# Optimization experiments

Measured on AMD Instinct MI355X. Metric: run time of the kernel, lower is better.

Reference implementation:

```python
import jax, jax.numpy as jnp
import numpy as np

N_NODES, N_EDGES, CH, FEAT = 20000, 320000, 256, 118


def setup_inputs() -> dict:
    key = jax.random.key(0)
    ks = jax.random.split(key, 8)
    x = jax.random.uniform(ks[0], (N_NODES, FEAT), dtype=jnp.float32)
    edge_index = jax.random.randint(ks[1], (2, N_EDGES), 0, N_NODES, dtype=jnp.int64)
    s = 0.05
    W_embed = jax.random.normal(ks[2], (FEAT, CH), dtype=jnp.float32) * s
    b_embed = jnp.zeros((CH,), jnp.float32)
    W1 = jax.random.normal(ks[3], (CH, CH), dtype=jnp.float32) * s
    b1 = jnp.zeros((CH,), jnp.float32)
    W2 = jax.random.normal(ks[4], (CH, CH), dtype=jnp.float32) * s
    b2 = jnp.zeros((CH,), jnp.float32)
    return {"x": x, "edge_index": edge_index, "W_embed": W_embed, "b_embed": b_embed,
            "W1": W1, "b1": b1, "W2": W2, "b2": b2}


def reference(x, edge_index, W_embed, b_embed, W1, b1, W2, b2):
    n = x.shape[0]
    # node embedding: Linear(118 -> C)
    h = x @ W_embed + b_embed  # [N, C]
    src, dst = edge_index[0], edge_index[1]
    # message: gather x_j per edge, dense1 + exact GELU (dropout = identity in eval)
    msg = jax.nn.gelu(h[src] @ W1 + b1, approximate=False)  # [E, C]
    # mean aggregation into destination nodes
    agg = jax.ops.segment_sum(msg, dst, num_segments=n)  # [N, C]
    cnt = jax.ops.segment_sum(jnp.ones((msg.shape[0],), msg.dtype), dst, num_segments=n)
    agg = agg / jnp.maximum(cnt, 1.0)[:, None]
    # update: dense2 + exact GELU
    out = jax.nn.gelu(agg @ W2 + b2, approximate=False)  # [N, C]
    # final mean over channel dim
    return out.mean(axis=1)  # [N]
```

## Files before the change

kernel.cpp:

```cpp
#include <hip/hip_runtime.h>
#include <math.h>

#define N_NODES 20000
#define N_EDGES 320000
#define CH      256
#define FEAT    118
#define CAP     48

typedef float    f32x4 __attribute__((ext_vector_type(4)));
typedef short    s16x8 __attribute__((ext_vector_type(8)));
typedef _Float16 f16x4 __attribute__((ext_vector_type(4)));
typedef _Float16 f16x8 __attribute__((ext_vector_type(8)));
typedef unsigned short u16;

union Frag  { s16x8 v; u16 u[8]; };
union FragH { f16x8 v; _Float16 h[8]; };

__device__ __forceinline__ float gelu_exact(float x) {
    return 0.5f * x * (1.0f + erff(x * 0.70710678118654752f));
}
__device__ __forceinline__ u16 f2bf(float f) {
    unsigned u = __float_as_uint(f);
    u = (u + 0x7FFFu + ((u >> 16) & 1u)) >> 16;
    return (u16)u;
}
__device__ __forceinline__ float bf2f(u16 h) { return __uint_as_float(((unsigned)h) << 16); }

__global__ __launch_bounds__(256) void prep(const float* __restrict__ x,
                                            const int* __restrict__ ei,
                                            const float* __restrict__ We,
                                            const float* __restrict__ be,
                                            const float* __restrict__ W1,
                                            const float* __restrict__ b1,
                                            const float* __restrict__ W2,
                                            u16* __restrict__ xh, u16* __restrict__ xl,
                                            int* __restrict__ cnt, int* __restrict__ bins,
                                            _Float16* __restrict__ w2h, _Float16* __restrict__ w2l,
                                            u16* __restrict__ wch, u16* __restrict__ wcl,
                                            float* __restrict__ bc) {
    const int b = blockIdx.x, tid = threadIdx.x;
    if (b < 1250) {
        __shared__ float xs[16][132];
        {
            int r = tid >> 4, ci = tid & 15;
            const float* xrow = x + (size_t)(b * 16 + r) * FEAT;
            #pragma unroll
            for (int it = 0; it < 8; it++) {
                int col = ci + it * 16;
                xs[r][col] = (col < FEAT) ? xrow[col] : 0.0f;
            }
        }
        __syncthreads();
        int lane = tid & 63, ks = tid >> 6;
        int row = lane & 15, k0 = ks * 32 + (lane >> 4) * 8;
        Frag hi, lo;
        #pragma unroll
        for (int j = 0; j < 8; j++) {
            float v = xs[row][k0 + j];
            u16 h = f2bf(v);
            hi.u[j] = h; lo.u[j] = f2bf(v - bf2f(h));
        }
        size_t fid = (size_t)b * 256 + tid;
        ((s16x8*)xh)[fid] = hi.v;
        ((s16x8*)xl)[fid] = lo.v;
    } else if (b < 2500) {
        int e = (b - 1250) * 256 + tid;
        int s = ei[e];
        int d = ei[N_EDGES + e];
        int p = atomicAdd(&cnt[d], 1);
        if (p < CAP) bins[(size_t)d * CAP + p] = s;
    } else if (b < 2532) {
        int fid = (b - 2500) * 256 + tid;
        int lane = fid & 63, ks = (fid >> 6) & 7, nt = fid >> 9;
        int n = nt * 16 + (lane & 15);
        int k0 = ks * 32 + (lane >> 4) * 8;
        FragH hi, lo;
        #pragma unroll
        for (int j = 0; j < 8; j++) {
            float v = W2[(size_t)(k0 + j) * 256 + n];
            _Float16 h = (_Float16)v;
            hi.h[j] = h;
            lo.h[j] = (_Float16)((v - (float)h) * 4096.0f);
        }
        ((f16x8*)w2h)[fid] = hi.v;
        ((f16x8*)w2l)[fid] = lo.v;
    } else {
        int f = b - 2532;
        int n = tid;
        if (f < 128) {
            float acc = 0.0f;
            if (f < FEAT) {
                const float* wr = We + (size_t)f * 256;
                #pragma unroll 8
                for (int c = 0; c < 256; c++) acc += wr[c] * W1[(size_t)c * 256 + n];
            }
            int nt = n >> 4, lm = n & 15, ks = f >> 5, q = (f >> 3) & 3, j = f & 7;
            size_t idx = (((size_t)nt * 4 + ks) * 64 + q * 16 + lm) * 8 + j;
            u16 h = f2bf(acc);
            wch[idx] = h;
            wcl[idx] = f2bf(acc - bf2f(h));
        } else {
            float acc = b1[n];
            #pragma unroll 8
            for (int c = 0; c < 256; c++) acc += be[c] * W1[(size_t)c * 256 + n];
            bc[n] = acc;
        }
    }
}

__global__ __launch_bounds__(256) void gemm_main(const u16* __restrict__ Ah_, const u16* __restrict__ Al_,
                                                 const u16* __restrict__ Bh_, const u16* __restrict__ Bl_,
                                                 const float* __restrict__ bias,
                                                 _Float16* __restrict__ Mout) {
    __shared__ _Float16 Ls[16][256];
    const int tid = threadIdx.x, wave = tid >> 6, lane = tid & 63;
    const int quad = lane >> 4, lm = lane & 15;
    const int mt = blockIdx.x, nt0 = wave * 4;
    const s16x8* Ah = (const s16x8*)Ah_; const s16x8* Al = (const s16x8*)Al_;
    const s16x8* Bh = (const s16x8*)Bh_; const s16x8* Bl = (const s16x8*)Bl_;
    f32x4 acc[4] = {f32x4{0,0,0,0}, f32x4{0,0,0,0}, f32x4{0,0,0,0}, f32x4{0,0,0,0}};
    #pragma unroll
    for (int ks = 0; ks < 4; ks++) {
        s16x8 a_h = Ah[((size_t)mt * 4 + ks) * 64 + lane];
        s16x8 a_l = Al[((size_t)mt * 4 + ks) * 64 + lane];
        #pragma unroll
        for (int t = 0; t < 4; t++) {
            s16x8 bh = Bh[((size_t)(nt0 + t) * 4 + ks) * 64 + lane];
            s16x8 bl = Bl[((size_t)(nt0 + t) * 4 + ks) * 64 + lane];
            acc[t] = __builtin_amdgcn_mfma_f32_16x16x32_bf16(a_h, bh, acc[t], 0, 0, 0);
            acc[t] = __builtin_amdgcn_mfma_f32_16x16x32_bf16(a_l, bh, acc[t], 0, 0, 0);
            acc[t] = __builtin_amdgcn_mfma_f32_16x16x32_bf16(a_h, bl, acc[t], 0, 0, 0);
        }
    }
    #pragma unroll
    for (int t = 0; t < 4; t++) {
        float bn = bias[(nt0 + t) * 16 + lm];
        #pragma unroll
        for (int r = 0; r < 4; r++)
            Ls[quad * 4 + r][(nt0 + t) * 16 + lm] = (_Float16)gelu_exact(acc[t][r] + bn);
    }
    __syncthreads();
    s16x8* dst = (s16x8*)Mout + (size_t)mt * 512;
    const s16x8* src = (const s16x8*)&Ls[0][0];
    dst[tid]       = src[tid];
    dst[256 + tid] = src[256 + tid];
}

__global__ __launch_bounds__(256) void aggregate(const _Float16* __restrict__ M,
                                                 const int* __restrict__ cnt,
                                                 const int* __restrict__ bins,
                                                 _Float16* __restrict__ aggf) {
    int node = (blockIdx.x * 256 + threadIdx.x) >> 6;
    int lane = threadIdx.x & 63;
    int c = cnt[node];
    int cc = min(c, CAP);
    int myid = (lane < CAP) ? bins[(size_t)node * CAP + lane] : 0;
    float a0 = 0.f, a1 = 0.f, a2 = 0.f, a3 = 0.f;
    for (int j = 0; j < cc; j += 8) {
        f16x4 v[8];
        #pragma unroll
        for (int u = 0; u < 8; u++) {
            int s = __shfl(myid, min(j + u, cc - 1), 64);
            v[u] = *(const f16x4*)(M + (size_t)s * CH + lane * 4);
        }
        #pragma unroll
        for (int u = 0; u < 8; u++) {
            if (j + u < cc) {
                a0 += (float)v[u].x; a1 += (float)v[u].y;
                a2 += (float)v[u].z; a3 += (float)v[u].w;
            }
        }
    }
    float inv = 1.0f / (float)max(c, 1);
    f16x4 o;
    o.x = (_Float16)(a0 * inv); o.y = (_Float16)(a1 * inv);
    o.z = (_Float16)(a2 * inv); o.w = (_Float16)(a3 * inv);
    int mt = node >> 4, lm = node & 15;
    int ks = lane >> 3, quad = (lane & 7) >> 1, j0 = (lane & 1) * 4;
    size_t base = (((size_t)mt * 8 + ks) * 64 + quad * 16 + lm) * 8 + j0;
    *(f16x4*)(aggf + base) = o;
}

__global__ __launch_bounds__(256) void gemm_mean(const _Float16* __restrict__ Af_,
                                                 const _Float16* __restrict__ Bh_, const _Float16* __restrict__ Bl_,
                                                 const float* __restrict__ bias,
                                                 float* __restrict__ out) {
    __shared__ float part[4][32];
    const int tid = threadIdx.x, wave = tid >> 6, lane = tid & 63;
    const int quad = lane >> 4, lm = lane & 15;
    const int mt0 = blockIdx.x * 2, nt0 = wave * 4;
    const f16x8* Af = (const f16x8*)Af_;
    const f16x8* Bh = (const f16x8*)Bh_; const f16x8* Bl = (const f16x8*)Bl_;
    f32x4 acch[2][4], accl[2][4];
    #pragma unroll
    for (int mi = 0; mi < 2; mi++)
        #pragma unroll
        for (int t = 0; t < 4; t++) {
            acch[mi][t] = f32x4{0.f, 0.f, 0.f, 0.f};
            accl[mi][t] = f32x4{0.f, 0.f, 0.f, 0.f};
        }
    #pragma unroll
    for (int ks = 0; ks < 8; ks++) {
        f16x8 a0 = Af[((size_t)(mt0 + 0) * 8 + ks) * 64 + lane];
        f16x8 a1 = Af[((size_t)(mt0 + 1) * 8 + ks) * 64 + lane];
        #pragma unroll
        for (int t = 0; t < 4; t++) {
            f16x8 bh = Bh[((size_t)(nt0 + t) * 8 + ks) * 64 + lane];
            f16x8 bl = Bl[((size_t)(nt0 + t) * 8 + ks) * 64 + lane];
            acch[0][t] = __builtin_amdgcn_mfma_f32_16x16x32_f16(a0, bh, acch[0][t], 0, 0, 0);
            accl[0][t] = __builtin_amdgcn_mfma_f32_16x16x32_f16(a0, bl, accl[0][t], 0, 0, 0);
            acch[1][t] = __builtin_amdgcn_mfma_f32_16x16x32_f16(a1, bh, acch[1][t], 0, 0, 0);
            accl[1][t] = __builtin_amdgcn_mfma_f32_16x16x32_f16(a1, bl, accl[1][t], 0, 0, 0);
        }
    }
    float p[2][4] = {{0.f,0.f,0.f,0.f},{0.f,0.f,0.f,0.f}};
    #pragma unroll
    for (int t = 0; t < 4; t++) {
        float bn = bias[(nt0 + t) * 16 + lm];
        #pragma unroll
        for (int mi = 0; mi < 2; mi++)
            #pragma unroll
            for (int r = 0; r < 4; r++)
                p[mi][r] += gelu_exact(acch[mi][t][r] + accl[mi][t][r] * (1.0f / 4096.0f) + bn);
    }
    #pragma unroll
    for (int off = 1; off < 16; off <<= 1)
        #pragma unroll
        for (int mi = 0; mi < 2; mi++)
            #pragma unroll
            for (int r = 0; r < 4; r++)
                p[mi][r] += __shfl_xor(p[mi][r], off, 64);
    if (lm == 0)
        #pragma unroll
        for (int mi = 0; mi < 2; mi++)
            #pragma unroll
            for (int r = 0; r < 4; r++)
                part[wave][mi * 16 + quad * 4 + r] = p[mi][r];
    __syncthreads();
    if (tid < 32) {
        float s = part[0][tid] + part[1][tid] + part[2][tid] + part[3][tid];
        out[blockIdx.x * 32 + tid] = s * (1.0f / 256.0f);
    }
}

extern "C" void kernel_launch(void* const* d_in, const int* in_sizes, int n_in,
                              void* d_out, int out_size, void* d_ws, size_t ws_size,
                              hipStream_t stream) {
    const float* x  = (const float*)d_in[0];
    const int*   ei = (const int*)d_in[1];
    const float* We = (const float*)d_in[2];
    const float* be = (const float*)d_in[3];
    const float* W1 = (const float*)d_in[4];
    const float* b1 = (const float*)d_in[5];
    const float* W2 = (const float*)d_in[6];
    const float* b2 = (const float*)d_in[7];
    float* out = (float*)d_out;

    char* ws = (char*)d_ws;
    size_t off = 0;
    u16* xh = (u16*)(ws + off);
    _Float16* aggf = (_Float16*)(ws + off);
    off += 5120000;
    u16* xl = (u16*)(ws + off); off += 5120000;
    _Float16* M = (_Float16*)(ws + off); off += 10240000;
    u16* wch = (u16*)(ws + off); off += 65536;
    u16* wcl = (u16*)(ws + off); off += 65536;
    _Float16* w2h = (_Float16*)(ws + off); off += 131072;
    _Float16* w2l = (_Float16*)(ws + off); off += 131072;
    float* bc = (float*)(ws + off); off += 1024;
    int* cnt  = (int*)(ws + off); off += N_NODES * 4;
    int* bins = (int*)(ws + off); off += (size_t)N_NODES * CAP * 4;

    hipMemsetAsync(cnt, 0, N_NODES * sizeof(int), stream);
    prep<<<2661, 256, 0, stream>>>(x, ei, We, be, W1, b1, W2,
                                   xh, xl, cnt, bins, w2h, w2l, wch, wcl, bc);
    gemm_main<<<N_NODES / 16, 256, 0, stream>>>(xh, xl, wch, wcl, bc, M);
    aggregate<<<N_NODES / 4, 256, 0, stream>>>(M, cnt, bins, aggf);
    gemm_mean<<<N_NODES / 32, 256, 0, stream>>>(aggf, w2h, w2l, b2, out);
}
```

Baseline: 151.7 us.

## Fuse all stages into one cooperative persistent kernel with grid syncs

Replaces the memset plus four kernel launches with a single cooperative kernel of 512 persistent blocks. The stages (prep, edge binning plus first GEMM, aggregation, second GEMM with mean) are separated by grid.sync, and each stage loops over virtual blocks. Edge binning now overlaps with the first GEMM, and aggregation handles two nodes per wave. The goal is to remove launch gaps and tail effects between kernels. The cost is grid-wide barriers and fixed occupancy, and the old kernels remain as a fallback if the cooperative launch fails.

```diff
diff --git a/kernel.cpp b/kernel.cpp
--- a/kernel.cpp
+++ b/kernel.cpp
@@ -1,11 +1,15 @@
 #include <hip/hip_runtime.h>
+#include <hip/hip_cooperative_groups.h>
 #include <math.h>
+
+namespace cg = cooperative_groups;
 
 #define N_NODES 20000
 #define N_EDGES 320000
 #define CH      256
 #define FEAT    118
 #define CAP     48
+#define GRID    512
 
 typedef float    f32x4 __attribute__((ext_vector_type(4)));
 typedef short    s16x8 __attribute__((ext_vector_type(8)));
@@ -25,6 +29,234 @@
     return (u16)u;
 }
 __device__ __forceinline__ float bf2f(u16 h) { return __uint_as_float(((unsigned)h) << 16); }
+
+struct MegaArgs {
+    const float* x; const int* ei;
+    const float* We; const float* be; const float* W1; const float* b1; const float* W2; const float* b2;
+    u16* xh; u16* xl;
+    int* cnt; int* bins;
+    _Float16* w2h; _Float16* w2l;
+    u16* wch; u16* wcl;
+    float* bc;
+    _Float16* M;
+    _Float16* aggf;
+    float* out;
+};
+
+__global__ __launch_bounds__(256, 2) void mega(MegaArgs a) {
+    cg::grid_group grid = cg::this_grid();
+    const int blk = blockIdx.x, tid = threadIdx.x;
+    const int wave = tid >> 6, lane = tid & 63;
+    const int quad = lane >> 4, lm = lane & 15;
+    __shared__ __align__(16) char shraw[16 * 132 * 4];
+
+    for (int g = blk * 256 + tid; g < N_NODES; g += GRID * 256)
+        a.cnt[g] = 0;
+    for (int vb = blk; vb < 1411; vb += GRID) {
+        if (vb < 1250) {
+            float (&xs)[16][132] = *reinterpret_cast<float (*)[16][132]>(shraw);
+            {
+                int r = tid >> 4, ci = tid & 15;
+                const float* xrow = a.x + (size_t)(vb * 16 + r) * FEAT;
+                #pragma unroll
+                for (int it = 0; it < 8; it++) {
+                    int col = ci + it * 16;
+                    xs[r][col] = (col < FEAT) ? xrow[col] : 0.0f;
+                }
+            }
+            __syncthreads();
+            int ks = wave;
+            int row = lane & 15, k0 = ks * 32 + (lane >> 4) * 8;
+            Frag hi, lo;
+            #pragma unroll
+            for (int j = 0; j < 8; j++) {
+                float v = xs[row][k0 + j];
+                u16 h = f2bf(v);
+                hi.u[j] = h; lo.u[j] = f2bf(v - bf2f(h));
+            }
+            size_t fid = (size_t)vb * 256 + tid;
+            ((s16x8*)a.xh)[fid] = hi.v;
+            ((s16x8*)a.xl)[fid] = lo.v;
+            __syncthreads();
+        } else if (vb < 1282) {
+            int fid = (vb - 1250) * 256 + tid;
+            int l = fid & 63, ks = (fid >> 6) & 7, nt = fid >> 9;
+            int n = nt * 16 + (l & 15);
+            int k0 = ks * 32 + (l >> 4) * 8;
+            FragH hi, lo;
+            #pragma unroll
+            for (int j = 0; j < 8; j++) {
+                float v = a.W2[(size_t)(k0 + j) * 256 + n];
+                _Float16 h = (_Float16)v;
+                hi.h[j] = h;
+                lo.h[j] = (_Float16)((v - (float)h) * 4096.0f);
+            }
+            ((f16x8*)a.w2h)[fid] = hi.v;
+            ((f16x8*)a.w2l)[fid] = lo.v;
+        } else {
+            int f = vb - 1282;
+            int n = tid;
+            if (f < 128) {
+                float acc = 0.0f;
+                if (f < FEAT) {
+                    const float* wr = a.We + (size_t)f * 256;
+                    #pragma unroll 8
+                    for (int c = 0; c < 256; c++) acc += wr[c] * a.W1[(size_t)c * 256 + n];
+                }
+                int nt = n >> 4, lm2 = n & 15, ks = f >> 5, q = (f >> 3) & 3, j = f & 7;
+                size_t idx = (((size_t)nt * 4 + ks) * 64 + q * 16 + lm2) * 8 + j;
+                u16 h = f2bf(acc);
+                a.wch[idx] = h;
+                a.wcl[idx] = f2bf(acc - bf2f(h));
+            } else {
+                float acc = a.b1[n];
+                #pragma unroll 8
+                for (int c = 0; c < 256; c++) acc += a.be[c] * a.W1[(size_t)c * 256 + n];
+                a.bc[n] = acc;
+            }
+        }
+    }
+    __threadfence();
+    grid.sync();
+
+    for (int vb = blk; vb < 2500; vb += GRID) {
+        if (vb < 1250) {
+            int e = vb * 256 + tid;
+            int s = a.ei[e];
+            int d = a.ei[N_EDGES + e];
+            int p = atomicAdd(&a.cnt[d], 1);
+            if (p < CAP) a.bins[(size_t)d * CAP + p] = s;
+        } else {
+            int mt = vb - 1250;
+            _Float16 (&Ls)[16][256] = *reinterpret_cast<_Float16 (*)[16][256]>(shraw);
+            const s16x8* Ah = (const s16x8*)a.xh; const s16x8* Al = (const s16x8*)a.xl;
+            const s16x8* Bh = (const s16x8*)a.wch; const s16x8* Bl = (const s16x8*)a.wcl;
+            const int nt0 = wave * 4;
+            f32x4 acc[4] = {f32x4{0,0,0,0}, f32x4{0,0,0,0}, f32x4{0,0,0,0}, f32x4{0,0,0,0}};
+            #pragma unroll
+            for (int ks = 0; ks < 4; ks++) {
+                s16x8 a_h = Ah[((size_t)mt * 4 + ks) * 64 + lane];
+                s16x8 a_l = Al[((size_t)mt * 4 + ks) * 64 + lane];
+                #pragma unroll
+                for (int t = 0; t < 4; t++) {
+                    s16x8 bh = Bh[((size_t)(nt0 + t) * 4 + ks) * 64 + lane];
+                    s16x8 bl = Bl[((size_t)(nt0 + t) * 4 + ks) * 64 + lane];
+                    acc[t] = __builtin_amdgcn_mfma_f32_16x16x32_bf16(a_h, bh, acc[t], 0, 0, 0);
+                    acc[t] = __builtin_amdgcn_mfma_f32_16x16x32_bf16(a_l, bh, acc[t], 0, 0, 0);
+                    acc[t] = __builtin_amdgcn_mfma_f32_16x16x32_bf16(a_h, bl, acc[t], 0, 0, 0);
+                }
+            }
+            #pragma unroll
+            for (int t = 0; t < 4; t++) {
+                float bn = a.bc[(nt0 + t) * 16 + lm];
+                #pragma unroll
+                for (int r = 0; r < 4; r++)
+                    Ls[quad * 4 + r][(nt0 + t) * 16 + lm] = (_Float16)gelu_exact(acc[t][r] + bn);
+            }
+            __syncthreads();
+            s16x8* dst = (s16x8*)a.M + (size_t)mt * 512;
+            const s16x8* src = (const s16x8*)&Ls[0][0];
+            dst[tid]       = src[tid];
+            dst[256 + tid] = src[256 + tid];
+            __syncthreads();
+        }
+    }
+    __threadfence();
+    grid.sync();
+
+    for (int nb = (blk * 4 + wave) * 2; nb < N_NODES; nb += GRID * 8) {
+        int c0 = a.cnt[nb],     cc0 = min(c0, CAP);
+        int c1 = a.cnt[nb + 1], cc1 = min(c1, CAP);
+        int id0 = (lane < CAP) ? a.bins[(size_t)nb * CAP + lane] : 0;
+        int id1 = (lane < CAP) ? a.bins[(size_t)(nb + 1) * CAP + lane] : 0;
+        float s0[4] = {0.f,0.f,0.f,0.f}, s1[4] = {0.f,0.f,0.f,0.f};
+        int mx = max(cc0, cc1);
+        for (int j = 0; j < mx; j += 8) {
+            f16x4 v0[8], v1[8];
+            #pragma unroll
+            for (int u = 0; u < 8; u++) {
+                int e0 = __shfl(id0, min(j + u, cc0 - 1), 64);
+                int e1 = __shfl(id1, min(j + u, cc1 - 1), 64);
+                v0[u] = *(const f16x4*)(a.M + (size_t)e0 * CH + lane * 4);
+                v1[u] = *(const f16x4*)(a.M + (size_t)e1 * CH + lane * 4);
+            }
+            #pragma unroll
+            for (int u = 0; u < 8; u++) {
+                if (j + u < cc0) {
+                    s0[0] += (float)v0[u].x; s0[1] += (float)v0[u].y;
+                    s0[2] += (float)v0[u].z; s0[3] += (float)v0[u].w;
+                }
+                if (j + u < cc1) {
+                    s1[0] += (float)v1[u].x; s1[1] += (float)v1[u].y;
+                    s1[2] += (float)v1[u].z; s1[3] += (float)v1[u].w;
+                }
+            }
+        }
+        int ks = lane >> 3, q2 = (lane & 7) >> 1, j0 = (lane & 1) * 4;
+        #pragma unroll
+        for (int which = 0; which < 2; which++) {
+            int node = nb + which;
+            int c = which ? c1 : c0;
+            float* s = which ? s1 : s0;
+            float inv = 1.0f / (float)max(c, 1);
+            f16x4 o;
+            o.x = (_Float16)(s[0] * inv); o.y = (_Float16)(s[1] * inv);
+            o.z = (_Float16)(s[2] * inv); o.w = (_Float16)(s[3] * inv);
+            int mt = node >> 4, lmn = node & 15;
+            size_t base = (((size_t)mt * 8 + ks) * 64 + q2 * 16 + lmn) * 8 + j0;
+            *(f16x4*)(a.aggf + base) = o;
+        }
+    }
+    __threadfence();
+    grid.sync();
+
+    for (int vb = blk; vb < 1250; vb += GRID) {
+        float (&part)[4][16] = *reinterpret_cast<float (*)[4][16]>(shraw);
+        const int mt = vb, nt0 = wave * 4;
+        const f16x8* Af = (const f16x8*)a.aggf;
+        const f16x8* Bh = (const f16x8*)a.w2h; const f16x8* Bl = (const f16x8*)a.w2l;
+        f32x4 acch[4], accl[4];
+        #pragma unroll
+        for (int t = 0; t < 4; t++) {
+            acch[t] = f32x4{0.f, 0.f, 0.f, 0.f};
+            accl[t] = f32x4{0.f, 0.f, 0.f, 0.f};
+        }
+        #pragma unroll
+        for (int ks = 0; ks < 8; ks++) {
+            f16x8 a0 = Af[((size_t)mt * 8 + ks) * 64 + lane];
+            #pragma unroll
+            for (int t = 0; t < 4; t++) {
+                f16x8 bh = Bh[((size_t)(nt0 + t) * 8 + ks) * 64 + lane];
+                f16x8 bl = Bl[((size_t)(nt0 + t) * 8 + ks) * 64 + lane];
+                acch[t] = __builtin_amdgcn_mfma_f32_16x16x32_f16(a0, bh, acch[t], 0, 0, 0);
+                accl[t] = __builtin_amdgcn_mfma_f32_16x16x32_f16(a0, bl, accl[t], 0, 0, 0);
+            }
+        }
+        float p[4] = {0.f, 0.f, 0.f, 0.f};
+        #pragma unroll
+        for (int t = 0; t < 4; t++) {
+            float bn = a.b2[(nt0 + t) * 16 + lm];
+            #pragma unroll
+            for (int r = 0; r < 4; r++)
+                p[r] += gelu_exact(acch[t][r] + accl[t][r] * (1.0f / 4096.0f) + bn);
+        }
+        #pragma unroll
+        for (int off = 1; off < 16; off <<= 1)
+            #pragma unroll
+            for (int r = 0; r < 4; r++)
+                p[r] += __shfl_xor(p[r], off, 64);
+        if (lm == 0)
+            #pragma unroll
+            for (int r = 0; r < 4; r++)
+                part[wave][quad * 4 + r] = p[r];
+        __syncthreads();
+        if (tid < 16) {
+            float s = part[0][tid] + part[1][tid] + part[2][tid] + part[3][tid];
+            a.out[mt * 16 + tid] = s * (1.0f / 256.0f);
+        }
+        __syncthreads();
+    }
+}
 
 __global__ __launch_bounds__(256) void prep(const float* __restrict__ x,
                                             const int* __restrict__ ei,
@@ -108,10 +340,10 @@
     }
 }
 
-__global__ __launch_bounds__(256) void gemm_main(const u16* __restrict__ Ah_, const u16* __restrict__ Al_,
-                                                 const u16* __restrict__ Bh_, const u16* __restrict__ Bl_,
-                                                 const float* __restrict__ bias,
-                                                 _Float16* __restrict__ Mout) {
+__global__ __launch_bounds__(256) void gemm_main_k(const u16* __restrict__ Ah_, const u16* __restrict__ Al_,
+                                                   const u16* __restrict__ Bh_, const u16* __restrict__ Bl_,
+                                                   const float* __restrict__ bias,
+                                                   _Float16* __restrict__ Mout) {
     __shared__ _Float16 Ls[16][256];
     const int tid = threadIdx.x, wave = tid >> 6, lane = tid & 63;
     const int quad = lane >> 4, lm = lane & 15;
@@ -146,10 +378,10 @@
     dst[256 + tid] = src[256 + tid];
 }
 
-__global__ __launch_bounds__(256) void aggregate(const _Float16* __restrict__ M,
-                                                 const int* __restrict__ cnt,
-                                                 const int* __restrict__ bins,
-                                                 _Float16* __restrict__ aggf) {
+__global__ __launch_bounds__(256) void aggregate_k(const _Float16* __restrict__ M,
+                                                   const int* __restrict__ cnt,
+                                                   const int* __restrict__ bins,
+                                                   _Float16* __restrict__ aggf) {
     int node = (blockIdx.x * 256 + threadIdx.x) >> 6;
     int lane = threadIdx.x & 63;
     int c = cnt[node];
@@ -181,10 +413,10 @@
     *(f16x4*)(aggf + base) = o;
 }
 
-__global__ __launch_bounds__(256) void gemm_mean(const _Float16* __restrict__ Af_,
-                                                 const _Float16* __restrict__ Bh_, const _Float16* __restrict__ Bl_,
-                                                 const float* __restrict__ bias,
-                                                 float* __restrict__ out) {
+__global__ __launch_bounds__(256) void gemm_mean_k(const _Float16* __restrict__ Af_,
+                                                   const _Float16* __restrict__ Bh_, const _Float16* __restrict__ Bl_,
+                                                   const float* __restrict__ bias,
+                                                   float* __restrict__ out) {
     __shared__ float part[4][32];
     const int tid = threadIdx.x, wave = tid >> 6, lane = tid & 63;
     const int quad = lane >> 4, lm = lane & 15;
@@ -246,16 +478,6 @@
 extern "C" void kernel_launch(void* const* d_in, const int* in_sizes, int n_in,
                               void* d_out, int out_size, void* d_ws, size_t ws_size,
                               hipStream_t stream) {
-    const float* x  = (const float*)d_in[0];
-    const int*   ei = (const int*)d_in[1];
-    const float* We = (const float*)d_in[2];
-    const float* be = (const float*)d_in[3];
-    const float* W1 = (const float*)d_in[4];
-    const float* b1 = (const float*)d_in[5];
-    const float* W2 = (const float*)d_in[6];
-    const float* b2 = (const float*)d_in[7];
-    float* out = (float*)d_out;
-
     char* ws = (char*)d_ws;
     size_t off = 0;
     u16* xh = (u16*)(ws + off);
@@ -271,10 +493,30 @@
     int* cnt  = (int*)(ws + off); off += N_NODES * 4;
     int* bins = (int*)(ws + off); off += (size_t)N_NODES * CAP * 4;
 
-    hipMemsetAsync(cnt, 0, N_NODES * sizeof(int), stream);
-    prep<<<2661, 256, 0, stream>>>(x, ei, We, be, W1, b1, W2,
-                                   xh, xl, cnt, bins, w2h, w2l, wch, wcl, bc);
-    gemm_main<<<N_NODES / 16, 256, 0, stream>>>(xh, xl, wch, wcl, bc, M);
-    aggregate<<<N_NODES / 4, 256, 0, stream>>>(M, cnt, bins, aggf);
-    gemm_mean<<<N_NODES / 32, 256, 0, stream>>>(aggf, w2h, w2l, b2, out);
-}
+    MegaArgs ma;
+    ma.x  = (const float*)d_in[0];
+    ma.ei = (const int*)d_in[1];
+    ma.We = (const float*)d_in[2];
+    ma.be = (const float*)d_in[3];
+    ma.W1 = (const float*)d_in[4];
+    ma.b1 = (const float*)d_in[5];
+    ma.W2 = (const float*)d_in[6];
+    ma.b2 = (const float*)d_in[7];
+    ma.xh = xh; ma.xl = xl; ma.cnt = cnt; ma.bins = bins;
+    ma.w2h = w2h; ma.w2l = w2l; ma.wch = wch; ma.wcl = wcl;
+    ma.bc = bc; ma.M = M; ma.aggf = aggf;
+    ma.out = (float*)d_out;
+
+    void* kp[] = { &ma };
+    hipError_t err = hipLaunchCooperativeKernel((void*)mega, dim3(GRID), dim3(256),
+                                                kp, 0, stream);
+    if (err != hipSuccess) {
+        (void)hipGetLastError();
+        (void)hipMemsetAsync(cnt, 0, N_NODES * sizeof(int), stream);
+        prep<<<2661, 256, 0, stream>>>(ma.x, ma.ei, ma.We, ma.be, ma.W1, ma.b1, ma.W2,
+                                       xh, xl, cnt, bins, w2h, w2l, wch, wcl, bc);
+        gemm_main_k<<<N_NODES / 16, 256, 0, stream>>>(xh, xl, wch, wcl, bc, M);
+        aggregate_k<<<N_NODES / 4, 256, 0, stream>>>(M, cnt, bins, aggf);
+        gemm_mean_k<<<N_NODES / 32, 256, 0, stream>>>(aggf, w2h, w2l, ma.b2, (float*)d_out);
+    }
+}
```

New measurement: 530.8 us. 3.5x slower.

## Move edge binning into main GEMM launch, fold memset into prep, shrink mean tile

Applied to the files above, without the earlier changes.

Edge binning with atomics moves out of the prep kernel and into extra blocks of the main GEMM launch, so it runs alongside the GEMM blocks. The separate memset of the count array is replaced by extra blocks in prep that zero it. The final GEMM+GELU+mean kernel now does one 16-row tile per block instead of two, doubling the block count to 1250. The aim is to drop one launch and spread work over more blocks, at the cost of less B-fragment reuse per block in the last kernel.

```diff
diff --git a/kernel.cpp b/kernel.cpp
--- a/kernel.cpp
+++ b/kernel.cpp
@@ -27,14 +27,13 @@
 __device__ __forceinline__ float bf2f(u16 h) { return __uint_as_float(((unsigned)h) << 16); }
 
 __global__ __launch_bounds__(256) void prep(const float* __restrict__ x,
-                                            const int* __restrict__ ei,
                                             const float* __restrict__ We,
                                             const float* __restrict__ be,
                                             const float* __restrict__ W1,
                                             const float* __restrict__ b1,
                                             const float* __restrict__ W2,
                                             u16* __restrict__ xh, u16* __restrict__ xl,
-                                            int* __restrict__ cnt, int* __restrict__ bins,
+                                            int* __restrict__ cnt,
                                             _Float16* __restrict__ w2h, _Float16* __restrict__ w2l,
                                             u16* __restrict__ wch, u16* __restrict__ wcl,
                                             float* __restrict__ bc) {
@@ -63,14 +62,8 @@
         size_t fid = (size_t)b * 256 + tid;
         ((s16x8*)xh)[fid] = hi.v;
         ((s16x8*)xl)[fid] = lo.v;
-    } else if (b < 2500) {
-        int e = (b - 1250) * 256 + tid;
-        int s = ei[e];
-        int d = ei[N_EDGES + e];
-        int p = atomicAdd(&cnt[d], 1);
-        if (p < CAP) bins[(size_t)d * CAP + p] = s;
-    } else if (b < 2532) {
-        int fid = (b - 2500) * 256 + tid;
+    } else if (b < 1282) {
+        int fid = (b - 1250) * 256 + tid;
         int lane = fid & 63, ks = (fid >> 6) & 7, nt = fid >> 9;
         int n = nt * 16 + (lane & 15);
         int k0 = ks * 32 + (lane >> 4) * 8;
@@ -84,8 +77,8 @@
         }
         ((f16x8*)w2h)[fid] = hi.v;
         ((f16x8*)w2l)[fid] = lo.v;
-    } else {
-        int f = b - 2532;
+    } else if (b < 1411) {
+        int f = b - 1282;
         int n = tid;
         if (f < 128) {
             float acc = 0.0f;
@@ -105,17 +98,31 @@
             for (int c = 0; c < 256; c++) acc += be[c] * W1[(size_t)c * 256 + n];
             bc[n] = acc;
         }
-    }
-}
-
-__global__ __launch_bounds__(256) void gemm_main(const u16* __restrict__ Ah_, const u16* __restrict__ Al_,
+    } else {
+        int g = (b - 1411) * 256 + tid;
+        if (g < N_NODES) cnt[g] = 0;
+    }
+}
+
+__global__ __launch_bounds__(256) void main_bins(const u16* __restrict__ Ah_, const u16* __restrict__ Al_,
                                                  const u16* __restrict__ Bh_, const u16* __restrict__ Bl_,
                                                  const float* __restrict__ bias,
+                                                 const int* __restrict__ ei,
+                                                 int* __restrict__ cnt, int* __restrict__ bins,
                                                  _Float16* __restrict__ Mout) {
+    const int b = blockIdx.x, tid = threadIdx.x;
+    if (b >= 1250) {
+        int e = (b - 1250) * 256 + tid;
+        int s = ei[e];
+        int d = ei[N_EDGES + e];
+        int p = atomicAdd(&cnt[d], 1);
+        if (p < CAP) bins[(size_t)d * CAP + p] = s;
+        return;
+    }
     __shared__ _Float16 Ls[16][256];
-    const int tid = threadIdx.x, wave = tid >> 6, lane = tid & 63;
+    const int wave = tid >> 6, lane = tid & 63;
     const int quad = lane >> 4, lm = lane & 15;
-    const int mt = blockIdx.x, nt0 = wave * 4;
+    const int mt = b, nt0 = wave * 4;
     const s16x8* Ah = (const s16x8*)Ah_; const s16x8* Al = (const s16x8*)Al_;
     const s16x8* Bh = (const s16x8*)Bh_; const s16x8* Bl = (const s16x8*)Bl_;
     f32x4 acc[4] = {f32x4{0,0,0,0}, f32x4{0,0,0,0}, f32x4{0,0,0,0}, f32x4{0,0,0,0}};
@@ -185,61 +192,50 @@
                                                  const _Float16* __restrict__ Bh_, const _Float16* __restrict__ Bl_,
                                                  const float* __restrict__ bias,
                                                  float* __restrict__ out) {
-    __shared__ float part[4][32];
+    __shared__ float part[4][16];
     const int tid = threadIdx.x, wave = tid >> 6, lane = tid & 63;
     const int quad = lane >> 4, lm = lane & 15;
-    const int mt0 = blockIdx.x * 2, nt0 = wave * 4;
+    const int mt = blockIdx.x, nt0 = wave * 4;
     const f16x8* Af = (const f16x8*)Af_;
     const f16x8* Bh = (const f16x8*)Bh_; const f16x8* Bl = (const f16x8*)Bl_;
-    f32x4 acch[2][4], accl[2][4];
-    #pragma unroll
-    for (int mi = 0; mi < 2; mi++)
-        #pragma unroll
-        for (int t = 0; t < 4; t++) {
-            acch[mi][t] = f32x4{0.f, 0.f, 0.f, 0.f};
-            accl[mi][t] = f32x4{0.f, 0.f, 0.f, 0.f};
-        }
+    f32x4 acch[4], accl[4];
+    #pragma unroll
+    for (int t = 0; t < 4; t++) {
+        acch[t] = f32x4{0.f, 0.f, 0.f, 0.f};
+        accl[t] = f32x4{0.f, 0.f, 0.f, 0.f};
+    }
     #pragma unroll
     for (int ks = 0; ks < 8; ks++) {
-        f16x8 a0 = Af[((size_t)(mt0 + 0) * 8 + ks) * 64 + lane];
-        f16x8 a1 = Af[((size_t)(mt0 + 1) * 8 + ks) * 64 + lane];
+        f16x8 a0 = Af[((size_t)mt * 8 + ks) * 64 + lane];
         #pragma unroll
         for (int t = 0; t < 4; t++) {
             f16x8 bh = Bh[((size_t)(nt0 + t) * 8 + ks) * 64 + lane];
             f16x8 bl = Bl[((size_t)(nt0 + t) * 8 + ks) * 64 + lane];
-            acch[0][t] = __builtin_amdgcn_mfma_f32_16x16x32_f16(a0, bh, acch[0][t], 0, 0, 0);
-            accl[0][t] = __builtin_amdgcn_mfma_f32_16x16x32_f16(a0, bl, accl[0][t], 0, 0, 0);
-            acch[1][t] = __builtin_amdgcn_mfma_f32_16x16x32_f16(a1, bh, acch[1][t], 0, 0, 0);
-            accl[1][t] = __builtin_amdgcn_mfma_f32_16x16x32_f16(a1, bl, accl[1][t], 0, 0, 0);
-        }
-    }
-    float p[2][4] = {{0.f,0.f,0.f,0.f},{0.f,0.f,0.f,0.f}};
+            acch[t] = __builtin_amdgcn_mfma_f32_16x16x32_f16(a0, bh, acch[t], 0, 0, 0);
+            accl[t] = __builtin_amdgcn_mfma_f32_16x16x32_f16(a0, bl, accl[t], 0, 0, 0);
+        }
+    }
+    float p[4] = {0.f, 0.f, 0.f, 0.f};
     #pragma unroll
     for (int t = 0; t < 4; t++) {
         float bn = bias[(nt0 + t) * 16 + lm];
         #pragma unroll
-        for (int mi = 0; mi < 2; mi++)
-            #pragma unroll
-            for (int r = 0; r < 4; r++)
-                p[mi][r] += gelu_exact(acch[mi][t][r] + accl[mi][t][r] * (1.0f / 4096.0f) + bn);
+        for (int r = 0; r < 4; r++)
+            p[r] += gelu_exact(acch[t][r] + accl[t][r] * (1.0f / 4096.0f) + bn);
     }
     #pragma unroll
     for (int off = 1; off < 16; off <<= 1)
         #pragma unroll
-        for (int mi = 0; mi < 2; mi++)
-            #pragma unroll
-            for (int r = 0; r < 4; r++)
-                p[mi][r] += __shfl_xor(p[mi][r], off, 64);
+        for (int r = 0; r < 4; r++)
+            p[r] += __shfl_xor(p[r], off, 64);
     if (lm == 0)
         #pragma unroll
-        for (int mi = 0; mi < 2; mi++)
-            #pragma unroll
-            for (int r = 0; r < 4; r++)
-                part[wave][mi * 16 + quad * 4 + r] = p[mi][r];
+        for (int r = 0; r < 4; r++)
+            part[wave][quad * 4 + r] = p[r];
     __syncthreads();
-    if (tid < 32) {
+    if (tid < 16) {
         float s = part[0][tid] + part[1][tid] + part[2][tid] + part[3][tid];
-        out[blockIdx.x * 32 + tid] = s * (1.0f / 256.0f);
+        out[mt * 16 + tid] = s * (1.0f / 256.0f);
     }
 }
 
@@ -271,10 +267,9 @@
     int* cnt  = (int*)(ws + off); off += N_NODES * 4;
     int* bins = (int*)(ws + off); off += (size_t)N_NODES * CAP * 4;
 
-    hipMemsetAsync(cnt, 0, N_NODES * sizeof(int), stream);
-    prep<<<2661, 256, 0, stream>>>(x, ei, We, be, W1, b1, W2,
-                                   xh, xl, cnt, bins, w2h, w2l, wch, wcl, bc);
-    gemm_main<<<N_NODES / 16, 256, 0, stream>>>(xh, xl, wch, wcl, bc, M);
+    prep<<<1490, 256, 0, stream>>>(x, We, be, W1, b1, W2,
+                                   xh, xl, cnt, w2h, w2l, wch, wcl, bc);
+    main_bins<<<2500, 256, 0, stream>>>(xh, xl, wch, wcl, bc, ei, cnt, bins, M);
     aggregate<<<N_NODES / 4, 256, 0, stream>>>(M, cnt, bins, aggf);
-    gemm_mean<<<N_NODES / 32, 256, 0, stream>>>(aggf, w2h, w2l, b2, out);
-}
+    gemm_mean<<<1250, 256, 0, stream>>>(aggf, w2h, w2l, b2, out);
+}
```

After: 153.3 us. Within noise of the previous version (+1.1%).

## Move edge binning into main GEMM launch, zero counts in prep, widen aggregate loads

Applied to the files above, without the earlier changes.

Edge binning (atomic scatter into per-destination bins) moves out of prep into extra blocks of the main GEMM kernel, so it can overlap with the MFMA work. The count-array memset is replaced by zeroing blocks inside prep, which removes one API call. The aggregate kernel now has each half-wave load 8 halfs per lane from a different neighbour and combines the halves with a cross-lane shuffle, giving wider loads and two rows in flight per instruction. The cost is a more heterogeneous main kernel and an extra reduction step in aggregate.

```diff
diff --git a/kernel.cpp b/kernel.cpp
--- a/kernel.cpp
+++ b/kernel.cpp
@@ -9,7 +9,6 @@
 
 typedef float    f32x4 __attribute__((ext_vector_type(4)));
 typedef short    s16x8 __attribute__((ext_vector_type(8)));
-typedef _Float16 f16x4 __attribute__((ext_vector_type(4)));
 typedef _Float16 f16x8 __attribute__((ext_vector_type(8)));
 typedef unsigned short u16;
 
@@ -27,14 +26,13 @@
 __device__ __forceinline__ float bf2f(u16 h) { return __uint_as_float(((unsigned)h) << 16); }
 
 __global__ __launch_bounds__(256) void prep(const float* __restrict__ x,
-                                            const int* __restrict__ ei,
                                             const float* __restrict__ We,
                                             const float* __restrict__ be,
                                             const float* __restrict__ W1,
                                             const float* __restrict__ b1,
                                             const float* __restrict__ W2,
                                             u16* __restrict__ xh, u16* __restrict__ xl,
-                                            int* __restrict__ cnt, int* __restrict__ bins,
+                                            int* __restrict__ cnt,
                                             _Float16* __restrict__ w2h, _Float16* __restrict__ w2l,
                                             u16* __restrict__ wch, u16* __restrict__ wcl,
                                             float* __restrict__ bc) {
@@ -63,14 +61,8 @@
         size_t fid = (size_t)b * 256 + tid;
         ((s16x8*)xh)[fid] = hi.v;
         ((s16x8*)xl)[fid] = lo.v;
-    } else if (b < 2500) {
-        int e = (b - 1250) * 256 + tid;
-        int s = ei[e];
-        int d = ei[N_EDGES + e];
-        int p = atomicAdd(&cnt[d], 1);
-        if (p < CAP) bins[(size_t)d * CAP + p] = s;
-    } else if (b < 2532) {
-        int fid = (b - 2500) * 256 + tid;
+    } else if (b < 1282) {
+        int fid = (b - 1250) * 256 + tid;
         int lane = fid & 63, ks = (fid >> 6) & 7, nt = fid >> 9;
         int n = nt * 16 + (lane & 15);
         int k0 = ks * 32 + (lane >> 4) * 8;
@@ -84,8 +76,8 @@
         }
         ((f16x8*)w2h)[fid] = hi.v;
         ((f16x8*)w2l)[fid] = lo.v;
-    } else {
-        int f = b - 2532;
+    } else if (b < 1411) {
+        int f = b - 1282;
         int n = tid;
         if (f < 128) {
             float acc = 0.0f;
@@ -105,17 +97,31 @@
             for (int c = 0; c < 256; c++) acc += be[c] * W1[(size_t)c * 256 + n];
             bc[n] = acc;
         }
-    }
-}
-
-__global__ __launch_bounds__(256) void gemm_main(const u16* __restrict__ Ah_, const u16* __restrict__ Al_,
+    } else {
+        int g = (b - 1411) * 256 + tid;
+        if (g < N_NODES) cnt[g] = 0;
+    }
+}
+
+__global__ __launch_bounds__(256) void main_bins(const u16* __restrict__ Ah_, const u16* __restrict__ Al_,
                                                  const u16* __restrict__ Bh_, const u16* __restrict__ Bl_,
                                                  const float* __restrict__ bias,
+                                                 const int* __restrict__ ei,
+                                                 int* __restrict__ cnt, int* __restrict__ bins,
                                                  _Float16* __restrict__ Mout) {
+    const int b = blockIdx.x, tid = threadIdx.x;
+    if (b >= 1250) {
+        int e = (b - 1250) * 256 + tid;
+        int s = ei[e];
+        int d = ei[N_EDGES + e];
+        int p = atomicAdd(&cnt[d], 1);
+        if (p < CAP) bins[(size_t)d * CAP + p] = s;
+        return;
+    }
     __shared__ _Float16 Ls[16][256];
-    const int tid = threadIdx.x, wave = tid >> 6, lane = tid & 63;
+    const int wave = tid >> 6, lane = tid & 63;
     const int quad = lane >> 4, lm = lane & 15;
-    const int mt = blockIdx.x, nt0 = wave * 4;
+    const int mt = b, nt0 = wave * 4;
     const s16x8* Ah = (const s16x8*)Ah_; const s16x8* Al = (const s16x8*)Al_;
     const s16x8* Bh = (const s16x8*)Bh_; const s16x8* Bl = (const s16x8*)Bl_;
     f32x4 acc[4] = {f32x4{0,0,0,0}, f32x4{0,0,0,0}, f32x4{0,0,0,0}, f32x4{0,0,0,0}};
@@ -152,33 +158,41 @@
                                                  _Float16* __restrict__ aggf) {
     int node = (blockIdx.x * 256 + threadIdx.x) >> 6;
     int lane = threadIdx.x & 63;
+    int half = lane >> 5, l32 = lane & 31;
     int c = cnt[node];
     int cc = min(c, CAP);
     int myid = (lane < CAP) ? bins[(size_t)node * CAP + lane] : 0;
-    float a0 = 0.f, a1 = 0.f, a2 = 0.f, a3 = 0.f;
+    float p[8] = {0.f, 0.f, 0.f, 0.f, 0.f, 0.f, 0.f, 0.f};
     for (int j = 0; j < cc; j += 8) {
-        f16x4 v[8];
-        #pragma unroll
-        for (int u = 0; u < 8; u++) {
-            int s = __shfl(myid, min(j + u, cc - 1), 64);
-            v[u] = *(const f16x4*)(M + (size_t)s * CH + lane * 4);
-        }
-        #pragma unroll
-        for (int u = 0; u < 8; u++) {
-            if (j + u < cc) {
-                a0 += (float)v[u].x; a1 += (float)v[u].y;
-                a2 += (float)v[u].z; a3 += (float)v[u].w;
-            }
-        }
-    }
-    float inv = 1.0f / (float)max(c, 1);
-    f16x4 o;
-    o.x = (_Float16)(a0 * inv); o.y = (_Float16)(a1 * inv);
-    o.z = (_Float16)(a2 * inv); o.w = (_Float16)(a3 * inv);
-    int mt = node >> 4, lm = node & 15;
-    int ks = lane >> 3, quad = (lane & 7) >> 1, j0 = (lane & 1) * 4;
-    size_t base = (((size_t)mt * 8 + ks) * 64 + quad * 16 + lm) * 8 + j0;
-    *(f16x4*)(aggf + base) = o;
+        f16x8 v[4];
+        float msk[4];
+        #pragma unroll
+        for (int u = 0; u < 4; u++) {
+            int jj = j + 2 * u + half;
+            int s = __shfl(myid, min(jj, cc - 1), 64);
+            v[u] = *(const f16x8*)(M + (size_t)s * CH + l32 * 8);
+            msk[u] = (jj < cc) ? 1.0f : 0.0f;
+        }
+        #pragma unroll
+        for (int u = 0; u < 4; u++)
+            #pragma unroll
+            for (int q = 0; q < 8; q++)
+                p[q] += msk[u] * (float)v[u][q];
+    }
+    #pragma unroll
+    for (int q = 0; q < 8; q++)
+        p[q] += __shfl_xor(p[q], 32, 64);
+    if (lane < 32) {
+        float inv = 1.0f / (float)max(c, 1);
+        FragH o;
+        #pragma unroll
+        for (int q = 0; q < 8; q++)
+            o.h[q] = (_Float16)(p[q] * inv);
+        int mt = node >> 4, lm = node & 15;
+        int ks = l32 >> 2, quad = l32 & 3;
+        size_t base = (((size_t)mt * 8 + ks) * 64 + quad * 16 + lm) * 8;
+        *(f16x8*)(aggf + base) = o.v;
+    }
 }
 
 __global__ __launch_bounds__(256) void gemm_mean(const _Float16* __restrict__ Af_,
@@ -271,10 +285,9 @@
     int* cnt  = (int*)(ws + off); off += N_NODES * 4;
     int* bins = (int*)(ws + off); off += (size_t)N_NODES * CAP * 4;
 
-    hipMemsetAsync(cnt, 0, N_NODES * sizeof(int), stream);
-    prep<<<2661, 256, 0, stream>>>(x, ei, We, be, W1, b1, W2,
-                                   xh, xl, cnt, bins, w2h, w2l, wch, wcl, bc);
-    gemm_main<<<N_NODES / 16, 256, 0, stream>>>(xh, xl, wch, wcl, bc, M);
+    prep<<<1490, 256, 0, stream>>>(x, We, be, W1, b1, W2,
+                                   xh, xl, cnt, w2h, w2l, wch, wcl, bc);
+    main_bins<<<2500, 256, 0, stream>>>(xh, xl, wch, wcl, bc, ei, cnt, bins, M);
     aggregate<<<N_NODES / 4, 256, 0, stream>>>(M, cnt, bins, aggf);
     gemm_mean<<<N_NODES / 32, 256, 0, stream>>>(aggf, w2h, w2l, b2, out);
 }
```

Measured after the change: 158.6 us. 1.05x slower.
